# Kernel tuning notes

Hardware: AMD Instinct MI355X
Metric: run time of the kernel (lower is better)

Reference implementation:

```python
import jax, jax.numpy as jnp
import numpy as np

N = 20000      # nodes
DEG = 16       # uniform in-degree (edges sorted by destination)
F_IN = 96      # raw node feature dim
T_EMB = 32     # node-type embedding dim -> conv1 input = 128
H = 128        # hidden_channels == out_channels
N_TYPES = 8


def _lstm_agg(x_seq, w_ih, w_hh, b_ih, b_hh):
    """LSTMAggregation: run LSTM over each node's neighbor sequence, return last hidden. x_seq: [N, T, F] -> [N, F]."""
    n = x_seq.shape[0]
    hdim = w_hh.shape[1]
    h0 = jnp.zeros((n, hdim), x_seq.dtype)
    bias = b_ih + b_hh

    def step(carry, x_t):
        h, c = carry
        gates = x_t @ w_ih.T + h @ w_hh.T + bias  # [N, 4H], torch gate order i,f,g,o
        i, f, g, o = jnp.split(gates, 4, axis=-1)
        i = jax.nn.sigmoid(i)
        f = jax.nn.sigmoid(f)
        g = jnp.tanh(g)
        o = jax.nn.sigmoid(o)
        c = f * c + i * g
        h = o * jnp.tanh(c)
        return (h, c), None

    (h, _), _ = jax.lax.scan(step, (h0, h0), jnp.swapaxes(x_seq, 0, 1))
    return h


def _sage_lstm(x, src, params):
    """SAGEConv with aggr='lstm': out = lin_l(LSTM_agg(x_j)) + lin_r(x)."""
    w_ih, w_hh, b_ih, b_hh, w_l, b_l, w_r = params
    # dst = repeat(arange(N), DEG) (sorted), so grouping neighbors per node is a reshape
    x_j = x[src].reshape(x.shape[0], DEG, x.shape[1])  # gather: [N, DEG, F]
    agg = _lstm_agg(x_j, w_ih, w_hh, b_ih, b_hh)
    return agg @ w_l.T + b_l + x @ w_r.T


def setup_inputs() -> dict:
    key = jax.random.key(0)
    ks = jax.random.split(key, 40)

    def rn(i, shape, s=0.05):
        return (jax.random.normal(ks[i], shape, jnp.float32) * s)

    inp = {
        "x": rn(0, (N, F_IN), 1.0),
        "node_type_ids": jax.random.randint(ks[1], (N,), 0, N_TYPES),
        "edge_src": jax.random.randint(ks[2], (N * DEG,), 0, N),
        "edge_dst": jnp.repeat(jnp.arange(N), DEG),
        "type_emb": rn(3, (N_TYPES, T_EMB)),
    }
    k = 4
    for l in (1, 2, 3):
        inp[f"w_ih{l}"] = rn(k, (4 * H, H)); k += 1
        inp[f"w_hh{l}"] = rn(k, (4 * H, H)); k += 1
        inp[f"b_ih{l}"] = rn(k, (4 * H,)); k += 1
        inp[f"b_hh{l}"] = rn(k, (4 * H,)); k += 1
        inp[f"w_l{l}"] = rn(k, (H, H)); k += 1
        inp[f"b_l{l}"] = rn(k, (H,)); k += 1
        inp[f"w_r{l}"] = rn(k, (H, H)); k += 1
    return inp


def reference(x, node_type_ids, edge_src, edge_dst, type_emb,
              w_ih1, w_hh1, b_ih1, b_hh1, w_l1, b_l1, w_r1,
              w_ih2, w_hh2, b_ih2, b_hh2, w_l2, b_l2, w_r2,
              w_ih3, w_hh3, b_ih3, b_hh3, w_l3, b_l3, w_r3):
    del edge_dst  # sortedness/uniform degree encoded in the reshape
    h = jnp.concatenate([x, type_emb[node_type_ids]], axis=1)  # [N, 128]
    h = jax.nn.relu(_sage_lstm(h, edge_src, (w_ih1, w_hh1, b_ih1, b_hh1, w_l1, b_l1, w_r1)))  # dropout = identity (eval)
    h = jax.nn.relu(_sage_lstm(h, edge_src, (w_ih2, w_hh2, b_ih2, b_hh2, w_l2, b_l2, w_r2)))
    h = _sage_lstm(h, edge_src, (w_ih3, w_hh3, b_ih3, b_hh3, w_l3, b_l3, w_r3))
    return h
```

## Files before the change

### kernel.cpp

```cpp
#include <hip/hip_runtime.h>

#define NN 20000
#define DEG 16
#define HDIM 128
#define GDIM 512

typedef __attribute__((ext_vector_type(8))) short bf16x8;
typedef __attribute__((ext_vector_type(4))) float f32x4;
typedef __attribute__((ext_vector_type(2))) unsigned u32x2;
typedef __attribute__((ext_vector_type(4))) unsigned u32x4;
typedef unsigned long long ull;

#define L2E  1.4426950408889634f
#define L2E2 2.8853900817779268f

__device__ __forceinline__ f32x4 mfma16(bf16x8 a, bf16x8 b, f32x4 c) {
    return __builtin_amdgcn_mfma_f32_16x16x32_bf16(a, b, c, 0, 0, 0);
}

__device__ __forceinline__ unsigned short f2bf(float f) {
    unsigned u = __builtin_bit_cast(unsigned, f);
    u += 0x7FFFu + ((u >> 16) & 1u);
    return (unsigned short)(u >> 16);
}

__device__ __forceinline__ unsigned cvtpk(float lo, float hi) {
    unsigned r;
    asm("v_cvt_pk_bf16_f32 %0, %1, %2" : "=v"(r) : "v"(lo), "v"(hi));
    return r;
}

__device__ __forceinline__ float bfhi(unsigned u) { return __builtin_bit_cast(float, u & 0xFFFF0000u); }
__device__ __forceinline__ float bflo(unsigned u) { return __builtin_bit_cast(float, u << 16); }

__device__ __forceinline__ void barrier_lgkm() {
    asm volatile("s_waitcnt lgkmcnt(0)\ns_barrier" ::: "memory");
}

__device__ __forceinline__ float sig_pre(float x) {
    return __builtin_amdgcn_rcpf(1.f + __builtin_amdgcn_exp2f(-x));
}
__device__ __forceinline__ float tanh_pre2(float x2) {
    return 1.f - 2.f * __builtin_amdgcn_rcpf(__builtin_amdgcn_exp2f(x2) + 1.f);
}

struct CvtArgs {
    const float *wih[3], *whh[3], *wl[3], *wr[3], *bih[3], *bhh[3];
    unsigned short *dih[3], *dhh[3], *dl[3], *dr[3];
    float *dbias[3];
};

__global__ __launch_bounds__(256) void cvt_kernel(CvtArgs a) {
    int l = blockIdx.x / 642, b = blockIdx.x % 642, t = threadIdx.x;
    if (b < 256) {
        int i = b * 256 + t;
        float s = ((i >> 14) == 2) ? L2E2 : L2E;
        a.dih[l][i] = f2bf(a.wih[l][i] * s);
    } else if (b < 512) {
        int i = (b - 256) * 256 + t;
        float s = ((i >> 14) == 2) ? L2E2 : L2E;
        a.dhh[l][i] = f2bf(a.whh[l][i] * s);
    } else if (b < 576) {
        int i = (b - 512) * 256 + t;
        a.dl[l][i] = f2bf(a.wl[l][i]);
    } else if (b < 640) {
        int i = (b - 576) * 256 + t;
        a.dr[l][i] = f2bf(a.wr[l][i]);
    } else {
        int i = (b - 640) * 256 + t;
        float s = ((i >> 7) == 2) ? L2E2 : L2E;
        a.dbias[l][i] = (a.bih[l][i] + a.bhh[l][i]) * s;
    }
}

__device__ __forceinline__ void phaseA2(const unsigned short (*htile)[136],
        const unsigned short* __restrict__ wih, const float* __restrict__ biasc,
        unsigned short* __restrict__ xihb, int mbase, int cl, int qh, int k8, int wv) {
    bf16x8 a0[4], a1[4];
#pragma unroll
    for (int kt = 0; kt < 4; ++kt) {
        a0[kt] = *(const bf16x8*)(&htile[cl][kt * 32 + k8]);
        a1[kt] = *(const bf16x8*)(&htile[16 + cl][kt * 32 + k8]);
    }
#pragma unroll
    for (int nt = 0; nt < 2; ++nt) {
        const int col = wv * 32 + nt * 16 + cl;
        f32x4 acc0[4], acc1[4];
#pragma unroll
        for (int g = 0; g < 4; ++g) {
            acc0[g] = (f32x4){0.f, 0.f, 0.f, 0.f};
            acc1[g] = (f32x4){0.f, 0.f, 0.f, 0.f};
        }
#pragma unroll
        for (int g = 0; g < 4; ++g)
#pragma unroll
            for (int kt = 0; kt < 4; ++kt) {
                bf16x8 b = *(const bf16x8*)(wih + (g * 128 + col) * HDIM + kt * 32 + k8);
                acc0[g] = mfma16(a0[kt], b, acc0[g]);
                acc1[g] = mfma16(a1[kt], b, acc1[g]);
            }
        float bias[4];
#pragma unroll
        for (int g = 0; g < 4; ++g) bias[g] = biasc[g * 128 + col];
#pragma unroll
        for (int r = 0; r < 4; ++r) {
            unsigned p0 = cvtpk(acc0[0][r] + bias[0], acc0[1][r] + bias[1]);
            unsigned p1 = cvtpk(acc0[2][r] + bias[2], acc0[3][r] + bias[3]);
            *(ull*)(xihb + (size_t)(mbase + qh * 4 + r) * GDIM + col * 4) =
                (ull)p0 | ((ull)p1 << 32);
            unsigned q0 = cvtpk(acc1[0][r] + bias[0], acc1[1][r] + bias[1]);
            unsigned q1 = cvtpk(acc1[2][r] + bias[2], acc1[3][r] + bias[3]);
            *(ull*)(xihb + (size_t)(mbase + 16 + qh * 4 + r) * GDIM + col * 4) =
                (ull)q0 | ((ull)q1 << 32);
        }
    }
}

__global__ __launch_bounds__(256) void gemmA0_kernel(
        const float* __restrict__ x, const int* __restrict__ types,
        const float* __restrict__ emb, const unsigned short* __restrict__ wih,
        const float* __restrict__ biasc, unsigned short* __restrict__ h0,
        unsigned short* __restrict__ xihb) {
    __shared__ unsigned short htile[32][136];
    const int tid = threadIdx.x;
    const int lane = tid & 63, wv = tid >> 6;
    const int cl = lane & 15, qh = lane >> 4, k8 = qh * 8;
    const int mbase = blockIdx.x * 32;

    const int row = tid >> 3, c0 = (tid & 7) * 16;
    f32x4 u[4];
    if (c0 < 96) {
#pragma unroll
        for (int j = 0; j < 4; ++j)
            u[j] = *(const f32x4*)(x + (size_t)(mbase + row) * 96 + c0 + 4 * j);
    } else {
        int ty = types[mbase + row];
#pragma unroll
        for (int j = 0; j < 4; ++j)
            u[j] = *(const f32x4*)(emb + ty * 32 + (c0 - 96) + 4 * j);
    }
    u32x4 pk, pk2;
    pk[0]  = cvtpk(u[0][0], u[0][1]); pk[1]  = cvtpk(u[0][2], u[0][3]);
    pk[2]  = cvtpk(u[1][0], u[1][1]); pk[3]  = cvtpk(u[1][2], u[1][3]);
    pk2[0] = cvtpk(u[2][0], u[2][1]); pk2[1] = cvtpk(u[2][2], u[2][3]);
    pk2[2] = cvtpk(u[3][0], u[3][1]); pk2[3] = cvtpk(u[3][2], u[3][3]);
    *(u32x4*)(&htile[row][c0]) = pk;
    *(u32x4*)(&htile[row][c0 + 8]) = pk2;
    *(u32x4*)(h0 + (size_t)(mbase + row) * HDIM + c0) = pk;
    *(u32x4*)(h0 + (size_t)(mbase + row) * HDIM + c0 + 8) = pk2;
    __syncthreads();

    phaseA2(htile, wih, biasc, xihb, mbase, cl, qh, k8, wv);
}

__global__ __launch_bounds__(512, 4) void lstm_kernel(
        const unsigned short* __restrict__ xihb, const unsigned short* __restrict__ whh,
        const int* __restrict__ esrc, unsigned short* __restrict__ agg) {
    __shared__ unsigned short hbuf[2][16][136];
    __shared__ unsigned srcs_t[256];

    const int tid = threadIdx.x;
    const int lane = tid & 63, wv = tid >> 6;
    const int cl = lane & 15, qh = lane >> 4, k8 = qh * 8;
    const int colb = wv * 16 + cl;
    const int base = blockIdx.x * 16;

    if (tid < 256)
        srcs_t[(tid & 15) * 16 + (tid >> 4)] = ((unsigned)esrc[base * DEG + tid]) << 10;

    bf16x8 bfr[4][4];
#pragma unroll
    for (int kt = 0; kt < 4; ++kt)
#pragma unroll
        for (int g = 0; g < 4; ++g)
            asm volatile("global_load_dwordx4 %0, %1, off"
                         : "=v"(bfr[kt][g])
                         : "v"(whh + (g * 128 + colb) * HDIM + kt * 32 + k8));
    asm volatile("s_waitcnt vmcnt(0)" ::: "memory");
    __builtin_amdgcn_sched_barrier(0);
    __syncthreads();

    const char* xb = (const char*)xihb;
    const unsigned coloff = (unsigned)colb * 8u;
    float c[4] = {};
    ull xA[4], xB[4];
    unsigned pk0 = 0, pk1 = 0;

    auto gath = [&](int t, ull* xr) {
        u32x4 sv = *(const u32x4*)&srcs_t[t * 16 + qh * 4];
        xr[0] = *(const ull*)(xb + (sv[0] | coloff));
        xr[1] = *(const ull*)(xb + (sv[1] | coloff));
        xr[2] = *(const ull*)(xb + (sv[2] | coloff));
        xr[3] = *(const ull*)(xb + (sv[3] | coloff));
    };
    gath(0, xA);
    gath(1, xB);

    auto step = [&](int t, ull* xu) {
        f32x4 acc[4];
#pragma unroll
        for (int r = 0; r < 4; ++r) {
            unsigned lo = (unsigned)xu[r], hi = (unsigned)(xu[r] >> 32);
            acc[0][r] = bflo(lo); acc[1][r] = bfhi(lo);
            acc[2][r] = bflo(hi); acc[3][r] = bfhi(hi);
        }
        if (t < 14) gath(t + 2, xu);
        if (t > 0) {
            const int rb = (t + 1) & 1;
            bf16x8 a[4];
#pragma unroll
            for (int kt = 0; kt < 4; ++kt)
                a[kt] = *(const bf16x8*)(&hbuf[rb][cl][kt * 32 + k8]);
#pragma unroll
            for (int g = 0; g < 4; ++g)
#pragma unroll
                for (int kt = 0; kt < 4; ++kt)
                    acc[g] = mfma16(a[kt], bfr[kt][g], acc[g]);
        }
        float hv[4];
#pragma unroll
        for (int r = 0; r < 4; ++r) {
            float is = sig_pre(acc[0][r]);
            float fs = sig_pre(acc[1][r]);
            float gt = tanh_pre2(acc[2][r]);
            float os = sig_pre(acc[3][r]);
            float cc = fs * c[r] + is * gt;
            c[r] = cc;
            hv[r] = os * tanh_pre2(cc * L2E2);
        }
        pk0 = cvtpk(hv[0], hv[1]);
        pk1 = cvtpk(hv[2], hv[3]);
        unsigned short* hp = &hbuf[t & 1][qh * 4][colb];
        hp[0]   = (unsigned short)pk0;
        hp[136] = (unsigned short)(pk0 >> 16);
        hp[272] = (unsigned short)pk1;
        hp[408] = (unsigned short)(pk1 >> 16);
        barrier_lgkm();
    };

#pragma unroll
    for (int tt = 0; tt < 8; ++tt) { step(2 * tt, xA); step(2 * tt + 1, xB); }

    unsigned short* ap = agg + (size_t)(base + qh * 4) * HDIM + colb;
    ap[0]   = (unsigned short)pk0;
    ap[128] = (unsigned short)(pk0 >> 16);
    ap[256] = (unsigned short)pk1;
    ap[384] = (unsigned short)(pk1 >> 16);
}

__global__ __launch_bounds__(256) void gemmCA_kernel(
        const unsigned short* __restrict__ agg, const unsigned short* __restrict__ hcur,
        const unsigned short* __restrict__ wl, const unsigned short* __restrict__ wr,
        const float* __restrict__ bl, const unsigned short* __restrict__ wih,
        const float* __restrict__ biasc, unsigned short* __restrict__ hnext,
        unsigned short* __restrict__ xihb) {
    __shared__ unsigned short htile[32][136];
    const int lane = threadIdx.x & 63, wv = threadIdx.x >> 6;
    const int cl = lane & 15, qh = lane >> 4, k8 = qh * 8;
    const int mbase = blockIdx.x * 32;

    bf16x8 bA0[4], bA1[4], bH0[4], bH1[4];
#pragma unroll
    for (int kt = 0; kt < 4; ++kt) {
        bA0[kt] = *(const bf16x8*)(agg  + (size_t)(mbase + cl) * HDIM + kt * 32 + k8);
        bA1[kt] = *(const bf16x8*)(agg  + (size_t)(mbase + 16 + cl) * HDIM + kt * 32 + k8);
        bH0[kt] = *(const bf16x8*)(hcur + (size_t)(mbase + cl) * HDIM + kt * 32 + k8);
        bH1[kt] = *(const bf16x8*)(hcur + (size_t)(mbase + 16 + cl) * HDIM + kt * 32 + k8);
    }
#pragma unroll
    for (int nt = 0; nt < 2; ++nt) {
        const int col = wv * 32 + nt * 16 + cl;
        f32x4 acc0 = {0.f, 0.f, 0.f, 0.f}, acc1 = {0.f, 0.f, 0.f, 0.f};
#pragma unroll
        for (int kt = 0; kt < 4; ++kt) {
            bf16x8 w = *(const bf16x8*)(wl + col * HDIM + kt * 32 + k8);
            acc0 = mfma16(bA0[kt], w, acc0);
            acc1 = mfma16(bA1[kt], w, acc1);
        }
#pragma unroll
        for (int kt = 0; kt < 4; ++kt) {
            bf16x8 w = *(const bf16x8*)(wr + col * HDIM + kt * 32 + k8);
            acc0 = mfma16(bH0[kt], w, acc0);
            acc1 = mfma16(bH1[kt], w, acc1);
        }
        float bias = bl[col];
#pragma unroll
        for (int r = 0; r < 4; ++r) {
            unsigned short v0 = f2bf(fmaxf(acc0[r] + bias, 0.f));
            unsigned short v1 = f2bf(fmaxf(acc1[r] + bias, 0.f));
            hnext[(size_t)(mbase + qh * 4 + r) * HDIM + col] = v0;
            hnext[(size_t)(mbase + 16 + qh * 4 + r) * HDIM + col] = v1;
            htile[qh * 4 + r][col] = v0;
            htile[16 + qh * 4 + r][col] = v1;
        }
    }
    __syncthreads();

    phaseA2(htile, wih, biasc, xihb, mbase, cl, qh, k8, wv);
}

__global__ __launch_bounds__(256) void gemmCF_kernel(
        const unsigned short* __restrict__ agg, const unsigned short* __restrict__ hcur,
        const unsigned short* __restrict__ wl, const unsigned short* __restrict__ wr,
        const float* __restrict__ bl, float* __restrict__ fout) {
    const int lane = threadIdx.x & 63, wv = threadIdx.x >> 6;
    const int cl = lane & 15, qh = lane >> 4, k8 = qh * 8;
    const int mbase = blockIdx.x * 32;

    bf16x8 bA0[4], bA1[4], bH0[4], bH1[4];
#pragma unroll
    for (int kt = 0; kt < 4; ++kt) {
        bA0[kt] = *(const bf16x8*)(agg  + (size_t)(mbase + cl) * HDIM + kt * 32 + k8);
        bA1[kt] = *(const bf16x8*)(agg  + (size_t)(mbase + 16 + cl) * HDIM + kt * 32 + k8);
        bH0[kt] = *(const bf16x8*)(hcur + (size_t)(mbase + cl) * HDIM + kt * 32 + k8);
        bH1[kt] = *(const bf16x8*)(hcur + (size_t)(mbase + 16 + cl) * HDIM + kt * 32 + k8);
    }
#pragma unroll
    for (int nt = 0; nt < 2; ++nt) {
        const int col = wv * 32 + nt * 16 + cl;
        f32x4 acc0 = {0.f, 0.f, 0.f, 0.f}, acc1 = {0.f, 0.f, 0.f, 0.f};
#pragma unroll
        for (int kt = 0; kt < 4; ++kt) {
            bf16x8 w = *(const bf16x8*)(wl + col * HDIM + kt * 32 + k8);
            acc0 = mfma16(bA0[kt], w, acc0);
            acc1 = mfma16(bA1[kt], w, acc1);
        }
#pragma unroll
        for (int kt = 0; kt < 4; ++kt) {
            bf16x8 w = *(const bf16x8*)(wr + col * HDIM + kt * 32 + k8);
            acc0 = mfma16(bH0[kt], w, acc0);
            acc1 = mfma16(bH1[kt], w, acc1);
        }
        float bias = bl[col];
#pragma unroll
        for (int r = 0; r < 4; ++r) {
            fout[(size_t)(mbase + qh * 4 + r) * HDIM + col] = acc0[r] + bias;
            fout[(size_t)(mbase + 16 + qh * 4 + r) * HDIM + col] = acc1[r] + bias;
        }
    }
}

extern "C" void kernel_launch(void* const* d_in, const int* in_sizes, int n_in,
                              void* d_out, int out_size, void* d_ws, size_t ws_size,
                              hipStream_t stream) {
    (void)in_sizes; (void)n_in; (void)out_size; (void)ws_size;

    const float* x     = (const float*)d_in[0];
    const int*   types = (const int*)d_in[1];
    const int*   esrc  = (const int*)d_in[2];
    const float* emb   = (const float*)d_in[4];

    char* ws = (char*)d_ws;
    unsigned short* hA   = (unsigned short*)ws; ws += (size_t)NN * HDIM * 2;
    unsigned short* hB   = (unsigned short*)ws; ws += (size_t)NN * HDIM * 2;
    unsigned short* agg  = (unsigned short*)ws; ws += (size_t)NN * HDIM * 2;
    unsigned short* xihb = (unsigned short*)ws; ws += (size_t)NN * GDIM * 2;
    unsigned short* wbf  = (unsigned short*)ws; ws += (size_t)3 * 163840 * 2;
    float*          bc   = (float*)ws;

    unsigned short *wihb[3], *whhb[3], *wlb[3], *wrb[3];
    float* bcl[3];
    CvtArgs ca;
    for (int l = 0; l < 3; ++l) {
        unsigned short* lb = wbf + (size_t)l * 163840;
        wihb[l] = lb;
        whhb[l] = lb + 65536;
        wlb[l]  = lb + 131072;
        wrb[l]  = lb + 147456;
        bcl[l]  = bc + l * 512;
        ca.wih[l] = (const float*)d_in[5 + 7 * l + 0];
        ca.whh[l] = (const float*)d_in[5 + 7 * l + 1];
        ca.bih[l] = (const float*)d_in[5 + 7 * l + 2];
        ca.bhh[l] = (const float*)d_in[5 + 7 * l + 3];
        ca.wl[l]  = (const float*)d_in[5 + 7 * l + 4];
        ca.wr[l]  = (const float*)d_in[5 + 7 * l + 6];
        ca.dih[l] = wihb[l]; ca.dhh[l] = whhb[l]; ca.dl[l] = wlb[l]; ca.dr[l] = wrb[l];
        ca.dbias[l] = bcl[l];
    }
    cvt_kernel<<<1926, 256, 0, stream>>>(ca);

    gemmA0_kernel<<<NN / 32, 256, 0, stream>>>(x, types, emb, wihb[0], bcl[0], hA, xihb);

    unsigned short* hc = hA;
    unsigned short* hn = hB;
    for (int l = 0; l < 3; ++l) {
        const float* bl = (const float*)d_in[5 + 7 * l + 5];
        lstm_kernel<<<NN / 16, 512, 0, stream>>>(xihb, whhb[l], esrc, agg);
        if (l < 2) {
            gemmCA_kernel<<<NN / 32, 256, 0, stream>>>(
                agg, hc, wlb[l], wrb[l], bl, wihb[l + 1], bcl[l + 1], hn, xihb);
            unsigned short* t = hc; hc = hn; hn = t;
        } else {
            gemmCF_kernel<<<NN / 32, 256, 0, stream>>>(
                agg, hc, wlb[l], wrb[l], bl, (float*)d_out);
        }
    }
}
```

Measured before the change: 303.5 us.

## Process 32 nodes per LSTM block and stream W_hh from global each step

The recurrent LSTM kernel now handles two 16-node sub-tiles per block, so each W_hh fragment feeds two MFMAs. The weights are no longer held in registers; they are re-read from global or L2 every time step. The grid is halved, the occupancy hint drops from 4 to 2, and the final step skips the shared-memory store and barrier. This trades register pressure and a smaller grid for more global weight traffic inside the serial recurrence.

```diff
diff --git a/kernel.cpp b/kernel.cpp
--- a/kernel.cpp
+++ b/kernel.cpp
@@ -153,99 +153,112 @@
     phaseA2(htile, wih, biasc, xihb, mbase, cl, qh, k8, wv);
 }
 
-__global__ __launch_bounds__(512, 4) void lstm_kernel(
+__global__ __launch_bounds__(512, 2) void lstm_kernel(
         const unsigned short* __restrict__ xihb, const unsigned short* __restrict__ whh,
         const int* __restrict__ esrc, unsigned short* __restrict__ agg) {
-    __shared__ unsigned short hbuf[2][16][136];
-    __shared__ unsigned srcs_t[256];
+    __shared__ unsigned short hbuf[2][32][136];
+    __shared__ unsigned srcs_t[512];
 
     const int tid = threadIdx.x;
     const int lane = tid & 63, wv = tid >> 6;
     const int cl = lane & 15, qh = lane >> 4, k8 = qh * 8;
     const int colb = wv * 16 + cl;
-    const int base = blockIdx.x * 16;
-
-    if (tid < 256)
-        srcs_t[(tid & 15) * 16 + (tid >> 4)] = ((unsigned)esrc[base * DEG + tid]) << 10;
-
-    bf16x8 bfr[4][4];
-#pragma unroll
-    for (int kt = 0; kt < 4; ++kt)
-#pragma unroll
-        for (int g = 0; g < 4; ++g)
-            asm volatile("global_load_dwordx4 %0, %1, off"
-                         : "=v"(bfr[kt][g])
-                         : "v"(whh + (g * 128 + colb) * HDIM + kt * 32 + k8));
-    asm volatile("s_waitcnt vmcnt(0)" ::: "memory");
-    __builtin_amdgcn_sched_barrier(0);
+    const int base = blockIdx.x * 32;
+
+    srcs_t[(tid & 15) * 32 + (tid >> 4)] = ((unsigned)esrc[base * DEG + tid]) << 10;
     __syncthreads();
 
-    const char* xb = (const char*)xihb;
-    const unsigned coloff = (unsigned)colb * 8u;
-    float c[4] = {};
-    ull xA[4], xB[4];
-    unsigned pk0 = 0, pk1 = 0;
-
-    auto gath = [&](int t, ull* xr) {
-        u32x4 sv = *(const u32x4*)&srcs_t[t * 16 + qh * 4];
-        xr[0] = *(const ull*)(xb + (sv[0] | coloff));
-        xr[1] = *(const ull*)(xb + (sv[1] | coloff));
-        xr[2] = *(const ull*)(xb + (sv[2] | coloff));
-        xr[3] = *(const ull*)(xb + (sv[3] | coloff));
-    };
-    gath(0, xA);
-    gath(1, xB);
-
-    auto step = [&](int t, ull* xu) {
-        f32x4 acc[4];
+    const unsigned short* wp = whh + colb * HDIM + k8;
+    const char* xp = (const char*)xihb + (size_t)colb * 8u;
+
+    float c[8];
+#pragma unroll
+    for (int i = 0; i < 8; ++i) c[i] = 0.f;
+    unsigned pk[4] = {0, 0, 0, 0};
+    ull xr[2][8];
+
+#pragma unroll
+    for (int s = 0; s < 2; ++s)
 #pragma unroll
         for (int r = 0; r < 4; ++r) {
-            unsigned lo = (unsigned)xu[r], hi = (unsigned)(xu[r] >> 32);
-            acc[0][r] = bflo(lo); acc[1][r] = bfhi(lo);
-            acc[2][r] = bflo(hi); acc[3][r] = bfhi(hi);
-        }
-        if (t < 14) gath(t + 2, xu);
+            xr[0][s * 4 + r] = *(const ull*)(xp + srcs_t[0 * 32 + s * 16 + qh * 4 + r]);
+            xr[1][s * 4 + r] = *(const ull*)(xp + srcs_t[1 * 32 + s * 16 + qh * 4 + r]);
+        }
+
+#pragma unroll
+    for (int t = 0; t < 16; ++t) {
+        f32x4 acc[2][4];
+#pragma unroll
+        for (int s = 0; s < 2; ++s)
+#pragma unroll
+            for (int r = 0; r < 4; ++r) {
+                unsigned lo = (unsigned)xr[t & 1][s * 4 + r];
+                unsigned hi = (unsigned)(xr[t & 1][s * 4 + r] >> 32);
+                acc[s][0][r] = bflo(lo); acc[s][1][r] = bfhi(lo);
+                acc[s][2][r] = bflo(hi); acc[s][3][r] = bfhi(hi);
+            }
+        if (t < 14) {
+#pragma unroll
+            for (int s = 0; s < 2; ++s)
+#pragma unroll
+                for (int r = 0; r < 4; ++r)
+                    xr[t & 1][s * 4 + r] =
+                        *(const ull*)(xp + srcs_t[(t + 2) * 32 + s * 16 + qh * 4 + r]);
+        }
         if (t > 0) {
             const int rb = (t + 1) & 1;
-            bf16x8 a[4];
-#pragma unroll
-            for (int kt = 0; kt < 4; ++kt)
-                a[kt] = *(const bf16x8*)(&hbuf[rb][cl][kt * 32 + k8]);
+            bf16x8 ha[4], hb[4];
+#pragma unroll
+            for (int kt = 0; kt < 4; ++kt) {
+                ha[kt] = *(const bf16x8*)(&hbuf[rb][cl][kt * 32 + k8]);
+                hb[kt] = *(const bf16x8*)(&hbuf[rb][16 + cl][kt * 32 + k8]);
+            }
 #pragma unroll
             for (int g = 0; g < 4; ++g)
 #pragma unroll
-                for (int kt = 0; kt < 4; ++kt)
-                    acc[g] = mfma16(a[kt], bfr[kt][g], acc[g]);
-        }
-        float hv[4];
-#pragma unroll
-        for (int r = 0; r < 4; ++r) {
-            float is = sig_pre(acc[0][r]);
-            float fs = sig_pre(acc[1][r]);
-            float gt = tanh_pre2(acc[2][r]);
-            float os = sig_pre(acc[3][r]);
-            float cc = fs * c[r] + is * gt;
-            c[r] = cc;
-            hv[r] = os * tanh_pre2(cc * L2E2);
-        }
-        pk0 = cvtpk(hv[0], hv[1]);
-        pk1 = cvtpk(hv[2], hv[3]);
-        unsigned short* hp = &hbuf[t & 1][qh * 4][colb];
-        hp[0]   = (unsigned short)pk0;
-        hp[136] = (unsigned short)(pk0 >> 16);
-        hp[272] = (unsigned short)pk1;
-        hp[408] = (unsigned short)(pk1 >> 16);
-        barrier_lgkm();
-    };
-
-#pragma unroll
-    for (int tt = 0; tt < 8; ++tt) { step(2 * tt, xA); step(2 * tt + 1, xB); }
-
-    unsigned short* ap = agg + (size_t)(base + qh * 4) * HDIM + colb;
-    ap[0]   = (unsigned short)pk0;
-    ap[128] = (unsigned short)(pk0 >> 16);
-    ap[256] = (unsigned short)pk1;
-    ap[384] = (unsigned short)(pk1 >> 16);
+                for (int kt = 0; kt < 4; ++kt) {
+                    bf16x8 w = *(const bf16x8*)(wp + (g * 128) * HDIM + kt * 32);
+                    acc[0][g] = mfma16(ha[kt], w, acc[0][g]);
+                    acc[1][g] = mfma16(hb[kt], w, acc[1][g]);
+                }
+        }
+#pragma unroll
+        for (int s = 0; s < 2; ++s) {
+            float hv[4];
+#pragma unroll
+            for (int r = 0; r < 4; ++r) {
+                float is = sig_pre(acc[s][0][r]);
+                float fs = sig_pre(acc[s][1][r]);
+                float gt = tanh_pre2(acc[s][2][r]);
+                float os = sig_pre(acc[s][3][r]);
+                float cc = fs * c[s * 4 + r] + is * gt;
+                c[s * 4 + r] = cc;
+                hv[r] = os * tanh_pre2(cc * L2E2);
+            }
+            pk[2 * s]     = cvtpk(hv[0], hv[1]);
+            pk[2 * s + 1] = cvtpk(hv[2], hv[3]);
+        }
+        if (t < 15) {
+#pragma unroll
+            for (int s = 0; s < 2; ++s) {
+                unsigned short* hp = &hbuf[t & 1][s * 16 + qh * 4][colb];
+                hp[0]   = (unsigned short)pk[2 * s];
+                hp[136] = (unsigned short)(pk[2 * s] >> 16);
+                hp[272] = (unsigned short)pk[2 * s + 1];
+                hp[408] = (unsigned short)(pk[2 * s + 1] >> 16);
+            }
+            barrier_lgkm();
+        }
+    }
+
+#pragma unroll
+    for (int s = 0; s < 2; ++s) {
+        unsigned short* ap = agg + (size_t)(base + s * 16 + qh * 4) * HDIM + colb;
+        ap[0]   = (unsigned short)pk[2 * s];
+        ap[128] = (unsigned short)(pk[2 * s] >> 16);
+        ap[256] = (unsigned short)pk[2 * s + 1];
+        ap[384] = (unsigned short)(pk[2 * s + 1] >> 16);
+    }
 }
 
 __global__ __launch_bounds__(256) void gemmCA_kernel(
@@ -385,7 +398,7 @@
     unsigned short* hn = hB;
     for (int l = 0; l < 3; ++l) {
         const float* bl = (const float*)d_in[5 + 7 * l + 5];
-        lstm_kernel<<<NN / 16, 512, 0, stream>>>(xihb, whhb[l], esrc, agg);
+        lstm_kernel<<<NN / 32, 512, 0, stream>>>(xihb, whhb[l], esrc, agg);
         if (l < 2) {
             gemmCA_kernel<<<NN / 32, 256, 0, stream>>>(
                 agg, hc, wlb[l], wrb[l], bl, wihb[l + 1], bcl[l + 1], hn, xihb);
```

Result: slower. 683.8 us (+125.3%).
